# Kernel optimization log

Hardware: AMD Instinct MI355X
Metric: run time of the kernel (lower is better)

Reference implementation:

```python
import jax, jax.numpy as jnp
import numpy as np

FC = 128      # feature_channels
P = 5         # patch_size
HID = 256     # hidden
OUT = 3       # out_channels
OMEGA = 30.0  # omega_0


def _siren_linear(key, fan_in, fan_out, first=False):
    kw, kb = jax.random.split(key)
    lim = (1.0 / fan_in) if first else (np.sqrt(6.0 / fan_in) / OMEGA)
    W = jax.random.uniform(kw, (fan_in, fan_out), jnp.float32, -lim, lim)
    b = jax.random.uniform(kb, (fan_out,), jnp.float32, -lim, lim)
    return W, b


def setup_inputs() -> dict:
    key = jax.random.key(0)
    ks = jax.random.split(key, 5)
    B, H, W = 2, 128, 128
    xi = jax.random.normal(ks[0], (B, FC, H, W), jnp.float32)
    in_dim = FC * P * P + 2  # 3202 = local patch features + (x, y) coords
    W0, b0 = _siren_linear(ks[1], in_dim, HID, first=True)
    W1, b1 = _siren_linear(ks[2], HID, HID)
    W2, b2 = _siren_linear(ks[3], HID, HID)
    W3, b3 = _siren_linear(ks[4], HID, OUT)
    return {"xi": xi, "W0": W0, "b0": b0, "W1": W1, "b1": b1,
            "W2": W2, "b2": b2, "W3": W3, "b3": b3}


def reference(xi, W0, b0, W1, b1, W2, b2, W3, b3):
    B, C, H, Wd = xi.shape
    # extract_local_encoding: 5x5 local patches per pixel, zero-padded ('SAME')
    patches = jax.lax.conv_general_dilated_patches(
        xi, filter_shape=(P, P), window_strides=(1, 1), padding="SAME")  # [B, C*P*P, H, W]
    local_enc = patches.transpose(0, 2, 3, 1).reshape(B * H * Wd, C * P * P)
    # make_coords: normalized pixel coords in [-1, 1]
    ys = jnp.linspace(-1.0, 1.0, H, dtype=xi.dtype)
    xs = jnp.linspace(-1.0, 1.0, Wd, dtype=xi.dtype)
    gy, gx = jnp.meshgrid(ys, xs, indexing="ij")
    coords = jnp.stack([gx, gy], axis=-1).reshape(1, H * Wd, 2)
    coords = jnp.broadcast_to(coords, (B, H * Wd, 2)).reshape(B * H * Wd, 2)
    x = jnp.concatenate([local_enc, coords], axis=-1)  # [N, 3202]
    # SIREN MLP: sin(omega_0 * (x W + b)) for 3 layers, linear head
    h = jnp.sin(OMEGA * (x @ W0 + b0))
    h = jnp.sin(OMEGA * (h @ W1 + b1))
    h = jnp.sin(OMEGA * (h @ W2 + b2))
    out = h @ W3 + b3                                   # [N, OUT]
    return out.reshape(B, H, Wd, OUT).transpose(0, 3, 1, 2)  # [B, OUT, H, W]
```

## Files before the change

kernel.cpp:

```cpp
#include <hip/hip_runtime.h>
#include <hip/hip_bf16.h>

typedef short bf16x8 __attribute__((ext_vector_type(8)));
typedef float f32x4 __attribute__((ext_vector_type(4)));
typedef int int4v __attribute__((ext_vector_type(4)));

#define OMEGA 30.0f

__device__ __forceinline__ float fast_sin30(float z) {
  float t = z * 4.7746483f;
  t = __builtin_amdgcn_fractf(t);
  return __builtin_amdgcn_sinf(t);
}

__global__ __launch_bounds__(256) void k_prep(const float* __restrict__ xi,
                                              const float* __restrict__ W0,
                                              const float* __restrict__ W1,
                                              const float* __restrict__ W2,
                                              __hip_bfloat16* __restrict__ xt,
                                              __hip_bfloat16* __restrict__ wt2,
                                              __hip_bfloat16* __restrict__ w1t,
                                              __hip_bfloat16* __restrict__ w2t) {
  __shared__ float tile[128][33];
  int bx = blockIdx.x, t = threadIdx.x;
  if (bx < 4096) {
    int b = bx >> 11, c0 = ((bx >> 9) & 3) << 5, hw0 = (bx & 511) << 5;
    int r = t >> 5, cc = t & 31;
    const float* src = xi + (((size_t)b * 128 + c0) << 14) + hw0;
#pragma unroll
    for (int i = 0; i < 4; ++i)
      tile[r + i * 8][cc] = src[(size_t)(r + i * 8) * 16384 + cc];
    __syncthreads();
    __hip_bfloat16* dst = xt + (((size_t)b * 16384 + hw0) << 7) + c0;
#pragma unroll
    for (int i = 0; i < 4; ++i)
      dst[(size_t)(r + i * 8) * 128 + cc] = __float2bfloat16(tile[cc][r + i * 8]);
  } else if (bx < 4296) {
    int q = bx - 4096, f = q >> 3, nb = q & 7;
    int nn = t & 31, cr = t >> 5;
#pragma unroll
    for (int i = 0; i < 16; ++i) {
      int c = cr * 16 + i;
      tile[c][nn] = W0[(size_t)(c * 25 + f) * 256 + nb * 32 + nn];
    }
    __syncthreads();
#pragma unroll
    for (int i = 0; i < 16; ++i) {
      int idx = i * 256 + t;
      int n = idx >> 7, c = idx & 127;
      wt2[(size_t)f * 32768 + (size_t)(nb * 32 + n) * 128 + c] = __float2bfloat16(tile[c][n]);
    }
  } else {
    int rI = bx - 4296;
    const float* src = (rI >> 6) ? W2 : W1;
    __hip_bfloat16* dst = (rI >> 6) ? w2t : w1t;
    int k0 = ((rI >> 3) & 7) << 5, n0 = (rI & 7) << 5;
    int r = t >> 5, cc = t & 31;
#pragma unroll
    for (int i = 0; i < 4; ++i)
      tile[r + i * 8][cc] = src[(size_t)(k0 + r + i * 8) * 256 + n0 + cc];
    __syncthreads();
#pragma unroll
    for (int i = 0; i < 4; ++i)
      dst[(size_t)(n0 + r + i * 8) * 256 + k0 + cc] = __float2bfloat16(tile[cc][r + i * 8]);
  }
}

__global__ __launch_bounds__(256) void k_conv(const __hip_bfloat16* __restrict__ xt,
                                              const __hip_bfloat16* __restrict__ wt2,
                                              const float* __restrict__ W0,
                                              const float* __restrict__ b0,
                                              __hip_bfloat16* __restrict__ h0) {
  __shared__ __align__(16) char Al[240 * 128];
  __shared__ __align__(16) char Bl[2][64 * 128];
  int tid = threadIdx.x;
  int bx = blockIdx.x;
  int b = bx >> 6, tr = (bx >> 3) & 7, tc = bx & 7;
  int n0 = blockIdx.y << 6;
  int lane = tid & 63, wave = tid >> 6;
  int lr = lane & 15, lg = lane >> 4;

  float wA[4], wB[4], bb[4];
#pragma unroll
  for (int ni = 0; ni < 4; ++ni) {
    int n = n0 + (ni << 4) + lr;
    wA[ni] = W0[3200 * 256 + n];
    wB[ni] = W0[3201 * 256 + n];
    bb[ni] = b0[n];
  }

  int4v breg[2];
  auto loadB = [&](int i) {
    int cb = (i / 25) & 1, f = i % 25;
#pragma unroll
    for (int j = 0; j < 2; ++j) {
      int idx = j * 256 + tid;
      int n = idx >> 3, s = idx & 7;
      breg[j] = *(const int4v*)(wt2 + (size_t)(f * 256 + n0 + n) * 128 + cb * 64 + s * 8);
    }
  };
  auto writeB = [&](int i) {
    char* dst = Bl[i & 1];
#pragma unroll
    for (int j = 0; j < 2; ++j) {
      int idx = j * 256 + tid;
      int n = idx >> 3, s = idx & 7;
      *(int4v*)(dst + n * 128 + ((s ^ (n & 7)) << 4)) = breg[j];
    }
  };

  loadB(0);
  writeB(0);
  loadB(1);

  f32x4 acc[2][4] = {};

  for (int rh = 0; rh < 2; ++rh) {
    for (int half = 0; half < 2; ++half) {
      __syncthreads();
#pragma unroll
      for (int ii = 0; ii < 8; ++ii) {
        int idx = ii * 256 + tid;
        if (idx < 1920) {
          int pos = idx >> 3, s = idx & 7;
          int py = pos / 20, px_ = pos - py * 20;
          int gh = (tr << 4) + (rh << 3) + py - 2, gw = (tc << 4) + px_ - 2;
          int4v v = {0, 0, 0, 0};
          if ((unsigned)gh < 128u && (unsigned)gw < 128u)
            v = *(const int4v*)(xt + (((size_t)((b << 14) + (gh << 7) + gw)) << 7) + half * 64 + s * 8);
          *(int4v*)(Al + pos * 128 + ((s ^ (pos & 7)) << 4)) = v;
        }
      }
      __syncthreads();

      for (int f = 0; f < 25; ++f) {
        int i = rh * 50 + half * 25 + f;
        if (i < 99) writeB(i + 1);
        if (i < 98) loadB(i + 2);
        int fy = f / 5, fx = f - fy * 5;
        int px = lr + fx;
        char* Bbuf = Bl[i & 1];
#pragma unroll
        for (int ks = 0; ks < 2; ++ks) {
          int sk = (ks << 2) + lg;
          bf16x8 a[2], bw[4];
#pragma unroll
          for (int mi = 0; mi < 2; ++mi) {
            int fl = wave + (mi << 2);
            int pos = (fl + fy) * 20 + px;
            a[mi] = *(const bf16x8*)(Al + pos * 128 + ((sk ^ (pos & 7)) << 4));
          }
#pragma unroll
          for (int ni = 0; ni < 4; ++ni) {
            int nr = (ni << 4) + lr;
            bw[ni] = *(const bf16x8*)(Bbuf + nr * 128 + ((sk ^ (nr & 7)) << 4));
          }
#pragma unroll
          for (int mi = 0; mi < 2; ++mi)
#pragma unroll
            for (int ni = 0; ni < 4; ++ni)
              acc[mi][ni] = __builtin_amdgcn_mfma_f32_16x16x32_bf16(a[mi], bw[ni], acc[mi][ni], 0, 0, 0);
        }
        __syncthreads();
      }
    }

    char* stg = Al + wave * 4096;
#pragma unroll
    for (int mi = 0; mi < 2; ++mi) {
      int fl = wave + (mi << 2);
      int H = (tr << 4) + (rh << 3) + fl;
      float gy = -1.f + (2.f / 127.f) * (float)H;
#pragma unroll
      for (int j = 0; j < 4; ++j) {
        int cpx = (lg << 2) + j;
        int W = (tc << 4) + cpx;
        float gx = -1.f + (2.f / 127.f) * (float)W;
#pragma unroll
        for (int ni = 0; ni < 4; ++ni) {
          float v = acc[mi][ni][j] + bb[ni] + gx * wA[ni] + gy * wB[ni];
          unsigned short bits = __hip_bfloat16_raw(__float2bfloat16(fast_sin30(v))).x;
          int n = (ni << 4) + lr;
          int c = n >> 3;
          *(unsigned short*)(stg + mi * 2048 + cpx * 128 + (((c ^ (cpx & 7)) << 4) | ((n & 7) << 1))) = bits;
        }
      }
    }
#pragma unroll
    for (int mi = 0; mi < 2; ++mi) {
      int fl = wave + (mi << 2);
      int H = (tr << 4) + (rh << 3) + fl;
#pragma unroll
      for (int i2 = 0; i2 < 2; ++i2) {
        int r = (i2 << 3) + (lane >> 3);
        int c = lane & 7;
        int4v v = *(const int4v*)(stg + mi * 2048 + r * 128 + ((c ^ (r & 7)) << 4));
        int m = (b << 14) + (H << 7) + (tc << 4) + r;
        *(int4v*)(h0 + (size_t)m * 256 + n0 + c * 8) = v;
      }
    }
    if (rh == 0) {
#pragma unroll
      for (int mi = 0; mi < 2; ++mi)
#pragma unroll
        for (int ni = 0; ni < 4; ++ni)
          acc[mi][ni] = f32x4{0.f, 0.f, 0.f, 0.f};
    }
  }
}

__global__ __launch_bounds__(256, 4) void k_fused(const __hip_bfloat16* __restrict__ h0,
                                                  const __hip_bfloat16* __restrict__ w1t,
                                                  const float* __restrict__ b1,
                                                  const __hip_bfloat16* __restrict__ w2t,
                                                  const float* __restrict__ b2,
                                                  const float* __restrict__ W3,
                                                  const float* __restrict__ b3,
                                                  float* __restrict__ out) {
  __shared__ __align__(16) char Hl[32 * 512];
  __shared__ float w3l[768];
  int tid = threadIdx.x;
  int m0 = blockIdx.x << 5;
  int lane = tid & 63, wave = tid >> 6;
  int lr = lane & 15, lg = lane >> 4;
  int mg = wave >> 1, nh = wave & 1;

  for (int i = tid; i < 768; i += 256) w3l[i] = W3[i];

  int mrow = m0 + (mg << 4) + lr;
  const char* pA0 = (const char*)(h0 + ((size_t)mrow << 8)) + (lg << 4);
  const char* pB1[8];
  const char* pB2[8];
  float bb1[8], bb2[8];
#pragma unroll
  for (int ni = 0; ni < 8; ++ni) {
    int n = (nh << 7) + (ni << 4) + lr;
    pB1[ni] = (const char*)(w1t + ((size_t)n << 8)) + (lg << 4);
    pB2[ni] = (const char*)(w2t + ((size_t)n << 8)) + (lg << 4);
    bb1[ni] = b1[n];
    bb2[ni] = b2[n];
  }

  f32x4 acc[8] = {};
#pragma unroll
  for (int ks = 0; ks < 8; ++ks) {
    bf16x8 a = *(const bf16x8*)(pA0 + ks * 64);
    bf16x8 bw[8];
#pragma unroll
    for (int ni = 0; ni < 8; ++ni) bw[ni] = *(const bf16x8*)(pB1[ni] + ks * 64);
#pragma unroll
    for (int ni = 0; ni < 8; ++ni)
      acc[ni] = __builtin_amdgcn_mfma_f32_16x16x32_bf16(a, bw[ni], acc[ni], 0, 0, 0);
  }
#pragma unroll
  for (int j = 0; j < 4; ++j) {
    int r = (mg << 4) + (lg << 2) + j;
#pragma unroll
    for (int ni = 0; ni < 8; ++ni) {
      int c = (nh << 7) + (ni << 4) + lr;
      unsigned short bits =
          __hip_bfloat16_raw(__float2bfloat16(fast_sin30(acc[ni][j] + bb1[ni]))).x;
      int sl = (c >> 3) ^ (r & 31);
      *(unsigned short*)(Hl + r * 512 + (sl << 4) + ((c & 7) << 1)) = bits;
    }
  }
  __syncthreads();

  int rA = (mg << 4) + lr;
  f32x4 acc2[8] = {};
#pragma unroll
  for (int ks = 0; ks < 8; ++ks) {
    int sk = (ks << 2) + lg;
    bf16x8 a = *(const bf16x8*)(Hl + rA * 512 + ((sk ^ (rA & 31)) << 4));
    bf16x8 bw[8];
#pragma unroll
    for (int ni = 0; ni < 8; ++ni) bw[ni] = *(const bf16x8*)(pB2[ni] + ks * 64);
#pragma unroll
    for (int ni = 0; ni < 8; ++ni)
      acc2[ni] = __builtin_amdgcn_mfma_f32_16x16x32_bf16(a, bw[ni], acc2[ni], 0, 0, 0);
  }
  __syncthreads();
#pragma unroll
  for (int j = 0; j < 4; ++j) {
    int r = (mg << 4) + (lg << 2) + j;
#pragma unroll
    for (int ni = 0; ni < 8; ++ni) {
      int c = (nh << 7) + (ni << 4) + lr;
      unsigned short bits =
          __hip_bfloat16_raw(__float2bfloat16(fast_sin30(acc2[ni][j] + bb2[ni]))).x;
      int sl = (c >> 3) ^ (r & 31);
      *(unsigned short*)(Hl + r * 512 + (sl << 4) + ((c & 7) << 1)) = bits;
    }
  }
  __syncthreads();

  int pix = tid >> 3, s = tid & 7;
  float a0 = 0.f, a1 = 0.f, a2 = 0.f;
#pragma unroll
  for (int q = 0; q < 4; ++q) {
    int sl = ((s << 2) + q) ^ (pix & 31);
    bf16x8 hv = *(const bf16x8*)(Hl + pix * 512 + (sl << 4));
#pragma unroll
    for (int e = 0; e < 8; ++e) {
      int k = (s << 5) + (q << 3) + e;
      float h = __uint_as_float((unsigned)(unsigned short)hv[e] << 16);
      a0 += h * w3l[k * 3 + 0];
      a1 += h * w3l[k * 3 + 1];
      a2 += h * w3l[k * 3 + 2];
    }
  }
#pragma unroll
  for (int d = 1; d < 8; d <<= 1) {
    a0 += __shfl_xor(a0, d);
    a1 += __shfl_xor(a1, d);
    a2 += __shfl_xor(a2, d);
  }
  if (s < 3) {
    int m = m0 + pix;
    int b = m >> 14, hw = m & 16383;
    float v = (s == 0) ? (a0 + b3[0]) : (s == 1) ? (a1 + b3[1]) : (a2 + b3[2]);
    out[((b * 3 + s) << 14) + hw] = v;
  }
}

extern "C" void kernel_launch(void* const* d_in, const int* in_sizes, int n_in,
                              void* d_out, int out_size, void* d_ws, size_t ws_size,
                              hipStream_t stream) {
  const float* xi = (const float*)d_in[0];
  const float* W0 = (const float*)d_in[1];
  const float* b0 = (const float*)d_in[2];
  const float* W1 = (const float*)d_in[3];
  const float* b1 = (const float*)d_in[4];
  const float* W2 = (const float*)d_in[5];
  const float* b2 = (const float*)d_in[6];
  const float* W3 = (const float*)d_in[7];
  const float* b3 = (const float*)d_in[8];
  float* out = (float*)d_out;
  char* ws = (char*)d_ws;

  __hip_bfloat16* xt  = (__hip_bfloat16*)(ws + 0);
  __hip_bfloat16* wt2 = (__hip_bfloat16*)(ws + 8388608);
  __hip_bfloat16* w1t = (__hip_bfloat16*)(ws + 10027008);
  __hip_bfloat16* w2t = (__hip_bfloat16*)(ws + 10158080);
  __hip_bfloat16* h0  = (__hip_bfloat16*)(ws + 10289152);

  k_prep<<<4424, 256, 0, stream>>>(xi, W0, W1, W2, xt, wt2, w1t, w2t);
  k_conv<<<dim3(128, 4), 256, 0, stream>>>(xt, wt2, W0, b0, h0);
  k_fused<<<1024, 256, 0, stream>>>(h0, w1t, b1, w2t, b2, W3, b3, out);
}
```

Measured before the change: 209.3 us.

## Merge three kernels into one persistent kernel with grid-wide barriers

Replaces the prep, conv and fused-MLP launches with a single 512-block kernel whose three phases are separated by an atomic-counter grid barrier, plus a tiny init kernel that resets the barrier. Each block does 8 transpose tiles in prep, one conv tile, and two 32-row MLP tiles. The aim is to cut launch gaps and tail effects between kernels. In exchange it relies on all 512 blocks being co-resident, which deadlocks if they are not, and it spends time spinning at the barriers. The MLP phase also loses the occupancy hint it had before, and the shared-memory footprint is sized for the largest phase.

```diff
diff --git a/kernel.cpp b/kernel.cpp
--- a/kernel.cpp
+++ b/kernel.cpp
@@ -6,6 +6,7 @@
 typedef int int4v __attribute__((ext_vector_type(4)));
 
 #define OMEGA 30.0f
+#define NBLK 512
 
 __device__ __forceinline__ float fast_sin30(float z) {
   float t = z * 4.7746483f;
@@ -13,313 +14,349 @@
   return __builtin_amdgcn_sinf(t);
 }
 
-__global__ __launch_bounds__(256) void k_prep(const float* __restrict__ xi,
+__device__ __forceinline__ void gbar(int* bar, int& mygen) {
+  __syncthreads();
+  if (threadIdx.x == 0) {
+    int g = mygen + 1;
+    if (__hip_atomic_fetch_add(&bar[0], 1, __ATOMIC_ACQ_REL, __HIP_MEMORY_SCOPE_AGENT) == NBLK - 1) {
+      __hip_atomic_store(&bar[0], 0, __ATOMIC_RELAXED, __HIP_MEMORY_SCOPE_AGENT);
+      __hip_atomic_store(&bar[16], g, __ATOMIC_RELEASE, __HIP_MEMORY_SCOPE_AGENT);
+    } else {
+      while (__hip_atomic_load(&bar[16], __ATOMIC_ACQUIRE, __HIP_MEMORY_SCOPE_AGENT) < g)
+        __builtin_amdgcn_s_sleep(2);
+    }
+    mygen = g;
+  }
+  __syncthreads();
+}
+
+__global__ void k_init(int* bar) {
+  bar[0] = 0;
+  bar[16] = 0;
+}
+
+__global__ __launch_bounds__(256) void k_mega(const float* __restrict__ xi,
                                               const float* __restrict__ W0,
+                                              const float* __restrict__ b0,
+                                              const float* __restrict__ b1,
+                                              const float* __restrict__ b2,
+                                              const float* __restrict__ W3,
+                                              const float* __restrict__ b3,
                                               const float* __restrict__ W1,
                                               const float* __restrict__ W2,
                                               __hip_bfloat16* __restrict__ xt,
                                               __hip_bfloat16* __restrict__ wt2,
                                               __hip_bfloat16* __restrict__ w1t,
-                                              __hip_bfloat16* __restrict__ w2t) {
-  __shared__ float tile[128][33];
-  int bx = blockIdx.x, t = threadIdx.x;
-  if (bx < 4096) {
-    int b = bx >> 11, c0 = ((bx >> 9) & 3) << 5, hw0 = (bx & 511) << 5;
-    int r = t >> 5, cc = t & 31;
-    const float* src = xi + (((size_t)b * 128 + c0) << 14) + hw0;
-#pragma unroll
-    for (int i = 0; i < 4; ++i)
-      tile[r + i * 8][cc] = src[(size_t)(r + i * 8) * 16384 + cc];
+                                              __hip_bfloat16* __restrict__ w2t,
+                                              __hip_bfloat16* __restrict__ h0,
+                                              float* __restrict__ out,
+                                              int* bar) {
+  __shared__ __align__(16) char SMEM[47104];
+  int bid = blockIdx.x;
+  int tid = threadIdx.x;
+  int mygen = 0;
+
+  {
+    float(*tile)[33] = reinterpret_cast<float(*)[33]>(SMEM);
+    int r = tid >> 5, cc = tid & 31;
+    for (int i8 = 0; i8 < 8; ++i8) {
+      int bx = (bid << 3) + i8;
+      int b = bx >> 11, c0 = ((bx >> 9) & 3) << 5, hw0 = (bx & 511) << 5;
+      const float* src = xi + (((size_t)b * 128 + c0) << 14) + hw0;
+      float v[4];
+#pragma unroll
+      for (int i = 0; i < 4; ++i) v[i] = src[(size_t)(r + i * 8) * 16384 + cc];
+      __syncthreads();
+#pragma unroll
+      for (int i = 0; i < 4; ++i) tile[r + i * 8][cc] = v[i];
+      __syncthreads();
+      __hip_bfloat16* dst = xt + (((size_t)b * 16384 + hw0) << 7) + c0;
+#pragma unroll
+      for (int i = 0; i < 4; ++i)
+        dst[(size_t)(r + i * 8) * 128 + cc] = __float2bfloat16(tile[cc][r + i * 8]);
+    }
     __syncthreads();
-    __hip_bfloat16* dst = xt + (((size_t)b * 16384 + hw0) << 7) + c0;
-#pragma unroll
-    for (int i = 0; i < 4; ++i)
-      dst[(size_t)(r + i * 8) * 128 + cc] = __float2bfloat16(tile[cc][r + i * 8]);
-  } else if (bx < 4296) {
-    int q = bx - 4096, f = q >> 3, nb = q & 7;
-    int nn = t & 31, cr = t >> 5;
-#pragma unroll
-    for (int i = 0; i < 16; ++i) {
-      int c = cr * 16 + i;
-      tile[c][nn] = W0[(size_t)(c * 25 + f) * 256 + nb * 32 + nn];
-    }
-    __syncthreads();
-#pragma unroll
-    for (int i = 0; i < 16; ++i) {
-      int idx = i * 256 + t;
-      int n = idx >> 7, c = idx & 127;
-      wt2[(size_t)f * 32768 + (size_t)(nb * 32 + n) * 128 + c] = __float2bfloat16(tile[c][n]);
-    }
-  } else {
-    int rI = bx - 4296;
-    const float* src = (rI >> 6) ? W2 : W1;
-    __hip_bfloat16* dst = (rI >> 6) ? w2t : w1t;
-    int k0 = ((rI >> 3) & 7) << 5, n0 = (rI & 7) << 5;
-    int r = t >> 5, cc = t & 31;
-#pragma unroll
-    for (int i = 0; i < 4; ++i)
-      tile[r + i * 8][cc] = src[(size_t)(k0 + r + i * 8) * 256 + n0 + cc];
-    __syncthreads();
-#pragma unroll
-    for (int i = 0; i < 4; ++i)
-      dst[(size_t)(n0 + r + i * 8) * 256 + k0 + cc] = __float2bfloat16(tile[cc][r + i * 8]);
+    if (bid < 200) {
+      int f = bid >> 3, nb = bid & 7;
+      int nn = tid & 31, cr = tid >> 5;
+#pragma unroll
+      for (int i = 0; i < 16; ++i) {
+        int c = cr * 16 + i;
+        tile[c][nn] = W0[(size_t)(c * 25 + f) * 256 + nb * 32 + nn];
+      }
+      __syncthreads();
+#pragma unroll
+      for (int i = 0; i < 16; ++i) {
+        int idx = i * 256 + tid;
+        int n = idx >> 7, c = idx & 127;
+        wt2[(size_t)f * 32768 + (size_t)(nb * 32 + n) * 128 + c] = __float2bfloat16(tile[c][n]);
+      }
+    } else if (bid < 328) {
+      int rI = bid - 200;
+      const float* src = (rI >> 6) ? W2 : W1;
+      __hip_bfloat16* dst = (rI >> 6) ? w2t : w1t;
+      int k0 = ((rI >> 3) & 7) << 5, n0 = (rI & 7) << 5;
+#pragma unroll
+      for (int i = 0; i < 4; ++i)
+        tile[r + i * 8][cc] = src[(size_t)(k0 + r + i * 8) * 256 + n0 + cc];
+      __syncthreads();
+#pragma unroll
+      for (int i = 0; i < 4; ++i)
+        dst[(size_t)(n0 + r + i * 8) * 256 + k0 + cc] = __float2bfloat16(tile[cc][r + i * 8]);
+    }
   }
-}
-
-__global__ __launch_bounds__(256) void k_conv(const __hip_bfloat16* __restrict__ xt,
-                                              const __hip_bfloat16* __restrict__ wt2,
-                                              const float* __restrict__ W0,
-                                              const float* __restrict__ b0,
-                                              __hip_bfloat16* __restrict__ h0) {
-  __shared__ __align__(16) char Al[240 * 128];
-  __shared__ __align__(16) char Bl[2][64 * 128];
-  int tid = threadIdx.x;
-  int bx = blockIdx.x;
-  int b = bx >> 6, tr = (bx >> 3) & 7, tc = bx & 7;
-  int n0 = blockIdx.y << 6;
-  int lane = tid & 63, wave = tid >> 6;
-  int lr = lane & 15, lg = lane >> 4;
-
-  float wA[4], wB[4], bb[4];
-#pragma unroll
-  for (int ni = 0; ni < 4; ++ni) {
-    int n = n0 + (ni << 4) + lr;
-    wA[ni] = W0[3200 * 256 + n];
-    wB[ni] = W0[3201 * 256 + n];
-    bb[ni] = b0[n];
+
+  gbar(bar, mygen);
+
+  {
+    char* Al = SMEM;
+    char* Bl = SMEM + 30720;
+    int bx = bid & 127;
+    int b = bx >> 6, tr = (bx >> 3) & 7, tc = bx & 7;
+    int n0 = (bid >> 7) << 6;
+    int lane = tid & 63, wave = tid >> 6;
+    int lr = lane & 15, lg = lane >> 4;
+
+    float wA[4], wB[4], bb[4];
+#pragma unroll
+    for (int ni = 0; ni < 4; ++ni) {
+      int n = n0 + (ni << 4) + lr;
+      wA[ni] = W0[3200 * 256 + n];
+      wB[ni] = W0[3201 * 256 + n];
+      bb[ni] = b0[n];
+    }
+
+    int4v breg[2];
+    auto loadB = [&](int i) {
+      int cb = (i / 25) & 1, f = i % 25;
+#pragma unroll
+      for (int j = 0; j < 2; ++j) {
+        int idx = j * 256 + tid;
+        int n = idx >> 3, s = idx & 7;
+        breg[j] = *(const int4v*)(wt2 + (size_t)(f * 256 + n0 + n) * 128 + cb * 64 + s * 8);
+      }
+    };
+    auto writeB = [&](int i) {
+      char* dst = Bl + (i & 1) * 8192;
+#pragma unroll
+      for (int j = 0; j < 2; ++j) {
+        int idx = j * 256 + tid;
+        int n = idx >> 3, s = idx & 7;
+        *(int4v*)(dst + n * 128 + ((s ^ (n & 7)) << 4)) = breg[j];
+      }
+    };
+
+    loadB(0);
+    writeB(0);
+    loadB(1);
+
+    f32x4 acc[2][4] = {};
+
+    for (int rh = 0; rh < 2; ++rh) {
+      for (int half = 0; half < 2; ++half) {
+        __syncthreads();
+#pragma unroll
+        for (int ii = 0; ii < 8; ++ii) {
+          int idx = ii * 256 + tid;
+          if (idx < 1920) {
+            int pos = idx >> 3, s = idx & 7;
+            int py = pos / 20, px_ = pos - py * 20;
+            int gh = (tr << 4) + (rh << 3) + py - 2, gw = (tc << 4) + px_ - 2;
+            int4v v = {0, 0, 0, 0};
+            if ((unsigned)gh < 128u && (unsigned)gw < 128u)
+              v = *(const int4v*)(xt + (((size_t)((b << 14) + (gh << 7) + gw)) << 7) + half * 64 + s * 8);
+            *(int4v*)(Al + pos * 128 + ((s ^ (pos & 7)) << 4)) = v;
+          }
+        }
+        __syncthreads();
+
+        for (int f = 0; f < 25; ++f) {
+          int i = rh * 50 + half * 25 + f;
+          if (i < 99) writeB(i + 1);
+          if (i < 98) loadB(i + 2);
+          int fy = f / 5, fx = f - fy * 5;
+          int px = lr + fx;
+          char* Bbuf = Bl + (i & 1) * 8192;
+#pragma unroll
+          for (int ks = 0; ks < 2; ++ks) {
+            int sk = (ks << 2) + lg;
+            bf16x8 a[2], bw[4];
+#pragma unroll
+            for (int mi = 0; mi < 2; ++mi) {
+              int fl = wave + (mi << 2);
+              int pos = (fl + fy) * 20 + px;
+              a[mi] = *(const bf16x8*)(Al + pos * 128 + ((sk ^ (pos & 7)) << 4));
+            }
+#pragma unroll
+            for (int ni = 0; ni < 4; ++ni) {
+              int nr = (ni << 4) + lr;
+              bw[ni] = *(const bf16x8*)(Bbuf + nr * 128 + ((sk ^ (nr & 7)) << 4));
+            }
+#pragma unroll
+            for (int mi = 0; mi < 2; ++mi)
+#pragma unroll
+              for (int ni = 0; ni < 4; ++ni)
+                acc[mi][ni] = __builtin_amdgcn_mfma_f32_16x16x32_bf16(a[mi], bw[ni], acc[mi][ni], 0, 0, 0);
+          }
+          __syncthreads();
+        }
+      }
+
+      char* stg = Al + wave * 4096;
+#pragma unroll
+      for (int mi = 0; mi < 2; ++mi) {
+        int fl = wave + (mi << 2);
+        int H = (tr << 4) + (rh << 3) + fl;
+        float gy = -1.f + (2.f / 127.f) * (float)H;
+#pragma unroll
+        for (int j = 0; j < 4; ++j) {
+          int cpx = (lg << 2) + j;
+          int W = (tc << 4) + cpx;
+          float gx = -1.f + (2.f / 127.f) * (float)W;
+#pragma unroll
+          for (int ni = 0; ni < 4; ++ni) {
+            float v = acc[mi][ni][j] + bb[ni] + gx * wA[ni] + gy * wB[ni];
+            unsigned short bits = __hip_bfloat16_raw(__float2bfloat16(fast_sin30(v))).x;
+            int n = (ni << 4) + lr;
+            int c = n >> 3;
+            *(unsigned short*)(stg + mi * 2048 + cpx * 128 + (((c ^ (cpx & 7)) << 4) | ((n & 7) << 1))) = bits;
+          }
+        }
+      }
+#pragma unroll
+      for (int mi = 0; mi < 2; ++mi) {
+        int fl = wave + (mi << 2);
+        int H = (tr << 4) + (rh << 3) + fl;
+#pragma unroll
+        for (int i2 = 0; i2 < 2; ++i2) {
+          int r2 = (i2 << 3) + (lane >> 3);
+          int c = lane & 7;
+          int4v v = *(const int4v*)(stg + mi * 2048 + r2 * 128 + ((c ^ (r2 & 7)) << 4));
+          int m = (b << 14) + (H << 7) + (tc << 4) + r2;
+          *(int4v*)(h0 + (size_t)m * 256 + n0 + c * 8) = v;
+        }
+      }
+      if (rh == 0) {
+#pragma unroll
+        for (int mi = 0; mi < 2; ++mi)
+#pragma unroll
+          for (int ni = 0; ni < 4; ++ni)
+            acc[mi][ni] = f32x4{0.f, 0.f, 0.f, 0.f};
+      }
+    }
   }
 
-  int4v breg[2];
-  auto loadB = [&](int i) {
-    int cb = (i / 25) & 1, f = i % 25;
-#pragma unroll
-    for (int j = 0; j < 2; ++j) {
-      int idx = j * 256 + tid;
-      int n = idx >> 3, s = idx & 7;
-      breg[j] = *(const int4v*)(wt2 + (size_t)(f * 256 + n0 + n) * 128 + cb * 64 + s * 8);
-    }
-  };
-  auto writeB = [&](int i) {
-    char* dst = Bl[i & 1];
-#pragma unroll
-    for (int j = 0; j < 2; ++j) {
-      int idx = j * 256 + tid;
-      int n = idx >> 3, s = idx & 7;
-      *(int4v*)(dst + n * 128 + ((s ^ (n & 7)) << 4)) = breg[j];
-    }
-  };
-
-  loadB(0);
-  writeB(0);
-  loadB(1);
-
-  f32x4 acc[2][4] = {};
-
-  for (int rh = 0; rh < 2; ++rh) {
-    for (int half = 0; half < 2; ++half) {
-      __syncthreads();
-#pragma unroll
-      for (int ii = 0; ii < 8; ++ii) {
-        int idx = ii * 256 + tid;
-        if (idx < 1920) {
-          int pos = idx >> 3, s = idx & 7;
-          int py = pos / 20, px_ = pos - py * 20;
-          int gh = (tr << 4) + (rh << 3) + py - 2, gw = (tc << 4) + px_ - 2;
-          int4v v = {0, 0, 0, 0};
-          if ((unsigned)gh < 128u && (unsigned)gw < 128u)
-            v = *(const int4v*)(xt + (((size_t)((b << 14) + (gh << 7) + gw)) << 7) + half * 64 + s * 8);
-          *(int4v*)(Al + pos * 128 + ((s ^ (pos & 7)) << 4)) = v;
-        }
-      }
-      __syncthreads();
-
-      for (int f = 0; f < 25; ++f) {
-        int i = rh * 50 + half * 25 + f;
-        if (i < 99) writeB(i + 1);
-        if (i < 98) loadB(i + 2);
-        int fy = f / 5, fx = f - fy * 5;
-        int px = lr + fx;
-        char* Bbuf = Bl[i & 1];
-#pragma unroll
-        for (int ks = 0; ks < 2; ++ks) {
-          int sk = (ks << 2) + lg;
-          bf16x8 a[2], bw[4];
-#pragma unroll
-          for (int mi = 0; mi < 2; ++mi) {
-            int fl = wave + (mi << 2);
-            int pos = (fl + fy) * 20 + px;
-            a[mi] = *(const bf16x8*)(Al + pos * 128 + ((sk ^ (pos & 7)) << 4));
-          }
-#pragma unroll
-          for (int ni = 0; ni < 4; ++ni) {
-            int nr = (ni << 4) + lr;
-            bw[ni] = *(const bf16x8*)(Bbuf + nr * 128 + ((sk ^ (nr & 7)) << 4));
-          }
-#pragma unroll
-          for (int mi = 0; mi < 2; ++mi)
-#pragma unroll
-            for (int ni = 0; ni < 4; ++ni)
-              acc[mi][ni] = __builtin_amdgcn_mfma_f32_16x16x32_bf16(a[mi], bw[ni], acc[mi][ni], 0, 0, 0);
-        }
-        __syncthreads();
-      }
-    }
-
-    char* stg = Al + wave * 4096;
-#pragma unroll
-    for (int mi = 0; mi < 2; ++mi) {
-      int fl = wave + (mi << 2);
-      int H = (tr << 4) + (rh << 3) + fl;
-      float gy = -1.f + (2.f / 127.f) * (float)H;
+  gbar(bar, mygen);
+
+  {
+    char* Hl = SMEM;
+    float* w3l = (float*)(SMEM + 16384);
+    int lane = tid & 63, wave = tid >> 6;
+    int lr = lane & 15, lg = lane >> 4;
+    int mg = wave >> 1, nh = wave & 1;
+
+    for (int i = tid; i < 768; i += 256) w3l[i] = W3[i];
+
+    const char* pB1[8];
+    const char* pB2[8];
+    float bb1[8], bb2[8];
+#pragma unroll
+    for (int ni = 0; ni < 8; ++ni) {
+      int n = (nh << 7) + (ni << 4) + lr;
+      pB1[ni] = (const char*)(w1t + ((size_t)n << 8)) + (lg << 4);
+      pB2[ni] = (const char*)(w2t + ((size_t)n << 8)) + (lg << 4);
+      bb1[ni] = b1[n];
+      bb2[ni] = b2[n];
+    }
+
+    for (int u = 0; u < 2; ++u) {
+      int m0 = ((bid << 1) + u) << 5;
+      __syncthreads();
+
+      int mrow = m0 + (mg << 4) + lr;
+      const char* pA0 = (const char*)(h0 + ((size_t)mrow << 8)) + (lg << 4);
+
+      f32x4 acc[8] = {};
+#pragma unroll
+      for (int ks = 0; ks < 8; ++ks) {
+        bf16x8 a = *(const bf16x8*)(pA0 + ks * 64);
+        bf16x8 bw[8];
+#pragma unroll
+        for (int ni = 0; ni < 8; ++ni) bw[ni] = *(const bf16x8*)(pB1[ni] + ks * 64);
+#pragma unroll
+        for (int ni = 0; ni < 8; ++ni)
+          acc[ni] = __builtin_amdgcn_mfma_f32_16x16x32_bf16(a, bw[ni], acc[ni], 0, 0, 0);
+      }
 #pragma unroll
       for (int j = 0; j < 4; ++j) {
-        int cpx = (lg << 2) + j;
-        int W = (tc << 4) + cpx;
-        float gx = -1.f + (2.f / 127.f) * (float)W;
-#pragma unroll
-        for (int ni = 0; ni < 4; ++ni) {
-          float v = acc[mi][ni][j] + bb[ni] + gx * wA[ni] + gy * wB[ni];
-          unsigned short bits = __hip_bfloat16_raw(__float2bfloat16(fast_sin30(v))).x;
-          int n = (ni << 4) + lr;
-          int c = n >> 3;
-          *(unsigned short*)(stg + mi * 2048 + cpx * 128 + (((c ^ (cpx & 7)) << 4) | ((n & 7) << 1))) = bits;
-        }
-      }
-    }
-#pragma unroll
-    for (int mi = 0; mi < 2; ++mi) {
-      int fl = wave + (mi << 2);
-      int H = (tr << 4) + (rh << 3) + fl;
-#pragma unroll
-      for (int i2 = 0; i2 < 2; ++i2) {
-        int r = (i2 << 3) + (lane >> 3);
-        int c = lane & 7;
-        int4v v = *(const int4v*)(stg + mi * 2048 + r * 128 + ((c ^ (r & 7)) << 4));
-        int m = (b << 14) + (H << 7) + (tc << 4) + r;
-        *(int4v*)(h0 + (size_t)m * 256 + n0 + c * 8) = v;
-      }
-    }
-    if (rh == 0) {
-#pragma unroll
-      for (int mi = 0; mi < 2; ++mi)
-#pragma unroll
-        for (int ni = 0; ni < 4; ++ni)
-          acc[mi][ni] = f32x4{0.f, 0.f, 0.f, 0.f};
-    }
-  }
-}
-
-__global__ __launch_bounds__(256, 4) void k_fused(const __hip_bfloat16* __restrict__ h0,
-                                                  const __hip_bfloat16* __restrict__ w1t,
-                                                  const float* __restrict__ b1,
-                                                  const __hip_bfloat16* __restrict__ w2t,
-                                                  const float* __restrict__ b2,
-                                                  const float* __restrict__ W3,
-                                                  const float* __restrict__ b3,
-                                                  float* __restrict__ out) {
-  __shared__ __align__(16) char Hl[32 * 512];
-  __shared__ float w3l[768];
-  int tid = threadIdx.x;
-  int m0 = blockIdx.x << 5;
-  int lane = tid & 63, wave = tid >> 6;
-  int lr = lane & 15, lg = lane >> 4;
-  int mg = wave >> 1, nh = wave & 1;
-
-  for (int i = tid; i < 768; i += 256) w3l[i] = W3[i];
-
-  int mrow = m0 + (mg << 4) + lr;
-  const char* pA0 = (const char*)(h0 + ((size_t)mrow << 8)) + (lg << 4);
-  const char* pB1[8];
-  const char* pB2[8];
-  float bb1[8], bb2[8];
-#pragma unroll
-  for (int ni = 0; ni < 8; ++ni) {
-    int n = (nh << 7) + (ni << 4) + lr;
-    pB1[ni] = (const char*)(w1t + ((size_t)n << 8)) + (lg << 4);
-    pB2[ni] = (const char*)(w2t + ((size_t)n << 8)) + (lg << 4);
-    bb1[ni] = b1[n];
-    bb2[ni] = b2[n];
-  }
-
-  f32x4 acc[8] = {};
-#pragma unroll
-  for (int ks = 0; ks < 8; ++ks) {
-    bf16x8 a = *(const bf16x8*)(pA0 + ks * 64);
-    bf16x8 bw[8];
-#pragma unroll
-    for (int ni = 0; ni < 8; ++ni) bw[ni] = *(const bf16x8*)(pB1[ni] + ks * 64);
-#pragma unroll
-    for (int ni = 0; ni < 8; ++ni)
-      acc[ni] = __builtin_amdgcn_mfma_f32_16x16x32_bf16(a, bw[ni], acc[ni], 0, 0, 0);
-  }
-#pragma unroll
-  for (int j = 0; j < 4; ++j) {
-    int r = (mg << 4) + (lg << 2) + j;
-#pragma unroll
-    for (int ni = 0; ni < 8; ++ni) {
-      int c = (nh << 7) + (ni << 4) + lr;
-      unsigned short bits =
-          __hip_bfloat16_raw(__float2bfloat16(fast_sin30(acc[ni][j] + bb1[ni]))).x;
-      int sl = (c >> 3) ^ (r & 31);
-      *(unsigned short*)(Hl + r * 512 + (sl << 4) + ((c & 7) << 1)) = bits;
-    }
-  }
-  __syncthreads();
-
-  int rA = (mg << 4) + lr;
-  f32x4 acc2[8] = {};
-#pragma unroll
-  for (int ks = 0; ks < 8; ++ks) {
-    int sk = (ks << 2) + lg;
-    bf16x8 a = *(const bf16x8*)(Hl + rA * 512 + ((sk ^ (rA & 31)) << 4));
-    bf16x8 bw[8];
-#pragma unroll
-    for (int ni = 0; ni < 8; ++ni) bw[ni] = *(const bf16x8*)(pB2[ni] + ks * 64);
-#pragma unroll
-    for (int ni = 0; ni < 8; ++ni)
-      acc2[ni] = __builtin_amdgcn_mfma_f32_16x16x32_bf16(a, bw[ni], acc2[ni], 0, 0, 0);
-  }
-  __syncthreads();
-#pragma unroll
-  for (int j = 0; j < 4; ++j) {
-    int r = (mg << 4) + (lg << 2) + j;
-#pragma unroll
-    for (int ni = 0; ni < 8; ++ni) {
-      int c = (nh << 7) + (ni << 4) + lr;
-      unsigned short bits =
-          __hip_bfloat16_raw(__float2bfloat16(fast_sin30(acc2[ni][j] + bb2[ni]))).x;
-      int sl = (c >> 3) ^ (r & 31);
-      *(unsigned short*)(Hl + r * 512 + (sl << 4) + ((c & 7) << 1)) = bits;
-    }
-  }
-  __syncthreads();
-
-  int pix = tid >> 3, s = tid & 7;
-  float a0 = 0.f, a1 = 0.f, a2 = 0.f;
-#pragma unroll
-  for (int q = 0; q < 4; ++q) {
-    int sl = ((s << 2) + q) ^ (pix & 31);
-    bf16x8 hv = *(const bf16x8*)(Hl + pix * 512 + (sl << 4));
-#pragma unroll
-    for (int e = 0; e < 8; ++e) {
-      int k = (s << 5) + (q << 3) + e;
-      float h = __uint_as_float((unsigned)(unsigned short)hv[e] << 16);
-      a0 += h * w3l[k * 3 + 0];
-      a1 += h * w3l[k * 3 + 1];
-      a2 += h * w3l[k * 3 + 2];
-    }
-  }
-#pragma unroll
-  for (int d = 1; d < 8; d <<= 1) {
-    a0 += __shfl_xor(a0, d);
-    a1 += __shfl_xor(a1, d);
-    a2 += __shfl_xor(a2, d);
-  }
-  if (s < 3) {
-    int m = m0 + pix;
-    int b = m >> 14, hw = m & 16383;
-    float v = (s == 0) ? (a0 + b3[0]) : (s == 1) ? (a1 + b3[1]) : (a2 + b3[2]);
-    out[((b * 3 + s) << 14) + hw] = v;
+        int r = (mg << 4) + (lg << 2) + j;
+#pragma unroll
+        for (int ni = 0; ni < 8; ++ni) {
+          int c = (nh << 7) + (ni << 4) + lr;
+          unsigned short bits =
+              __hip_bfloat16_raw(__float2bfloat16(fast_sin30(acc[ni][j] + bb1[ni]))).x;
+          int sl = (c >> 3) ^ (r & 31);
+          *(unsigned short*)(Hl + r * 512 + (sl << 4) + ((c & 7) << 1)) = bits;
+        }
+      }
+      __syncthreads();
+
+      int rA = (mg << 4) + lr;
+      f32x4 acc2[8] = {};
+#pragma unroll
+      for (int ks = 0; ks < 8; ++ks) {
+        int sk = (ks << 2) + lg;
+        bf16x8 a = *(const bf16x8*)(Hl + rA * 512 + ((sk ^ (rA & 31)) << 4));
+        bf16x8 bw[8];
+#pragma unroll
+        for (int ni = 0; ni < 8; ++ni) bw[ni] = *(const bf16x8*)(pB2[ni] + ks * 64);
+#pragma unroll
+        for (int ni = 0; ni < 8; ++ni)
+          acc2[ni] = __builtin_amdgcn_mfma_f32_16x16x32_bf16(a, bw[ni], acc2[ni], 0, 0, 0);
+      }
+      __syncthreads();
+#pragma unroll
+      for (int j = 0; j < 4; ++j) {
+        int r = (mg << 4) + (lg << 2) + j;
+#pragma unroll
+        for (int ni = 0; ni < 8; ++ni) {
+          int c = (nh << 7) + (ni << 4) + lr;
+          unsigned short bits =
+              __hip_bfloat16_raw(__float2bfloat16(fast_sin30(acc2[ni][j] + bb2[ni]))).x;
+          int sl = (c >> 3) ^ (r & 31);
+          *(unsigned short*)(Hl + r * 512 + (sl << 4) + ((c & 7) << 1)) = bits;
+        }
+      }
+      __syncthreads();
+
+      int pix = tid >> 3, s = tid & 7;
+      float a0 = 0.f, a1 = 0.f, a2 = 0.f;
+#pragma unroll
+      for (int q = 0; q < 4; ++q) {
+        int sl = ((s << 2) + q) ^ (pix & 31);
+        bf16x8 hv = *(const bf16x8*)(Hl + pix * 512 + (sl << 4));
+#pragma unroll
+        for (int e = 0; e < 8; ++e) {
+          int k = (s << 5) + (q << 3) + e;
+          float h = __uint_as_float((unsigned)(unsigned short)hv[e] << 16);
+          a0 += h * w3l[k * 3 + 0];
+          a1 += h * w3l[k * 3 + 1];
+          a2 += h * w3l[k * 3 + 2];
+        }
+      }
+#pragma unroll
+      for (int d = 1; d < 8; d <<= 1) {
+        a0 += __shfl_xor(a0, d);
+        a1 += __shfl_xor(a1, d);
+        a2 += __shfl_xor(a2, d);
+      }
+      if (s < 3) {
+        int m = m0 + pix;
+        int b = m >> 14, hw = m & 16383;
+        float v = (s == 0) ? (a0 + b3[0]) : (s == 1) ? (a1 + b3[1]) : (a2 + b3[2]);
+        out[((b * 3 + s) << 14) + hw] = v;
+      }
+    }
   }
 }
 
@@ -343,8 +380,9 @@
   __hip_bfloat16* w1t = (__hip_bfloat16*)(ws + 10027008);
   __hip_bfloat16* w2t = (__hip_bfloat16*)(ws + 10158080);
   __hip_bfloat16* h0  = (__hip_bfloat16*)(ws + 10289152);
-
-  k_prep<<<4424, 256, 0, stream>>>(xi, W0, W1, W2, xt, wt2, w1t, w2t);
-  k_conv<<<dim3(128, 4), 256, 0, stream>>>(xt, wt2, W0, b0, h0);
-  k_fused<<<1024, 256, 0, stream>>>(h0, w1t, b1, w2t, b2, W3, b3, out);
-}
+  int* bar            = (int*)(ws + 27066368);
+
+  k_init<<<1, 1, 0, stream>>>(bar);
+  k_mega<<<NBLK, 256, 0, stream>>>(xi, W0, b0, b1, b2, W3, b3, W1, W2,
+                                   xt, wt2, w1t, w2t, h0, out, bar);
+}
```

Result: slower. 352.2 us (+68.3%).

## Stage two filter taps per barrier in conv and vectorize prep transposes

Applied to the files above, without the earlier changes.

The conv kernel now loads and double-buffers the B weights for two filter taps per pipeline step, which halves the number of __syncthreads barriers in the inner loop at the cost of doubling the B LDS buffer. The prep kernel handles all 128 channels per block and writes 16-byte bf16x8 vectors instead of scalar bf16 stores. This cuts its grid from 4424 to 1352 blocks and coalesces its writes. The tap-pair indexing uses multiply-shift divisions, and the odd final tap of each 25-tap group is handled separately.

```diff
diff --git a/kernel.cpp b/kernel.cpp
--- a/kernel.cpp
+++ b/kernel.cpp
@@ -11,6 +11,10 @@
   float t = z * 4.7746483f;
   t = __builtin_amdgcn_fractf(t);
   return __builtin_amdgcn_sinf(t);
+}
+
+__device__ __forceinline__ unsigned short f2bf(float x) {
+  return __hip_bfloat16_raw(__float2bfloat16(x)).x;
 }
 
 __global__ __launch_bounds__(256) void k_prep(const float* __restrict__ xi,
@@ -21,48 +25,61 @@
                                               __hip_bfloat16* __restrict__ wt2,
                                               __hip_bfloat16* __restrict__ w1t,
                                               __hip_bfloat16* __restrict__ w2t) {
-  __shared__ float tile[128][33];
-  int bx = blockIdx.x, t = threadIdx.x;
-  if (bx < 4096) {
-    int b = bx >> 11, c0 = ((bx >> 9) & 3) << 5, hw0 = (bx & 511) << 5;
-    int r = t >> 5, cc = t & 31;
-    const float* src = xi + (((size_t)b * 128 + c0) << 14) + hw0;
-#pragma unroll
-    for (int i = 0; i < 4; ++i)
-      tile[r + i * 8][cc] = src[(size_t)(r + i * 8) * 16384 + cc];
-    __syncthreads();
-    __hip_bfloat16* dst = xt + (((size_t)b * 16384 + hw0) << 7) + c0;
-#pragma unroll
-    for (int i = 0; i < 4; ++i)
-      dst[(size_t)(r + i * 8) * 128 + cc] = __float2bfloat16(tile[cc][r + i * 8]);
-  } else if (bx < 4296) {
-    int q = bx - 4096, f = q >> 3, nb = q & 7;
-    int nn = t & 31, cr = t >> 5;
+  __shared__ float lds[128][33];
+  int bid = blockIdx.x, t = threadIdx.x;
+  if (bid < 1024) {
+    int b = bid >> 9, hw0 = (bid & 511) << 5;
+    int cc = t & 31, cr = t >> 5;
 #pragma unroll
     for (int i = 0; i < 16; ++i) {
       int c = cr * 16 + i;
-      tile[c][nn] = W0[(size_t)(c * 25 + f) * 256 + nb * 32 + nn];
-    }
-    __syncthreads();
+      lds[c][cc] = xi[(((size_t)(b * 128 + c)) << 14) + hw0 + cc];
+    }
+    __syncthreads();
+    int cg = t & 15;
+#pragma unroll
+    for (int it = 0; it < 2; ++it) {
+      int hw = (t >> 4) + (it << 4);
+      bf16x8 v;
+#pragma unroll
+      for (int w = 0; w < 8; ++w) v[w] = (short)f2bf(lds[cg * 8 + w][hw]);
+      *(bf16x8*)(xt + (((size_t)((b << 14) + hw0 + hw)) << 7) + cg * 8) = v;
+    }
+  } else if (bid < 1224) {
+    int q = bid - 1024, f = q >> 3, nb = q & 7;
+    int nn = t & 31, cr = t >> 5;
 #pragma unroll
     for (int i = 0; i < 16; ++i) {
-      int idx = i * 256 + t;
-      int n = idx >> 7, c = idx & 127;
-      wt2[(size_t)f * 32768 + (size_t)(nb * 32 + n) * 128 + c] = __float2bfloat16(tile[c][n]);
+      int c = cr * 16 + i;
+      lds[c][nn] = W0[(size_t)(c * 25 + f) * 256 + nb * 32 + nn];
+    }
+    __syncthreads();
+    int cg = t & 15;
+#pragma unroll
+    for (int it = 0; it < 2; ++it) {
+      int n = (t >> 4) + (it << 4);
+      bf16x8 v;
+#pragma unroll
+      for (int w = 0; w < 8; ++w) v[w] = (short)f2bf(lds[cg * 8 + w][n]);
+      *(bf16x8*)(wt2 + (size_t)f * 32768 + (size_t)(nb * 32 + n) * 128 + cg * 8) = v;
     }
   } else {
-    int rI = bx - 4296;
+    int rI = bid - 1224;
     const float* src = (rI >> 6) ? W2 : W1;
     __hip_bfloat16* dst = (rI >> 6) ? w2t : w1t;
     int k0 = ((rI >> 3) & 7) << 5, n0 = (rI & 7) << 5;
-    int r = t >> 5, cc = t & 31;
+    int cc = t & 31, r = t >> 5;
 #pragma unroll
     for (int i = 0; i < 4; ++i)
-      tile[r + i * 8][cc] = src[(size_t)(k0 + r + i * 8) * 256 + n0 + cc];
-    __syncthreads();
-#pragma unroll
-    for (int i = 0; i < 4; ++i)
-      dst[(size_t)(n0 + r + i * 8) * 256 + k0 + cc] = __float2bfloat16(tile[cc][r + i * 8]);
+      lds[r + i * 8][cc] = src[(size_t)(k0 + r + i * 8) * 256 + n0 + cc];
+    __syncthreads();
+    if (t < 128) {
+      int kg = t & 3, n = t >> 2;
+      bf16x8 v;
+#pragma unroll
+      for (int w = 0; w < 8; ++w) v[w] = (short)f2bf(lds[kg * 8 + w][n]);
+      *(bf16x8*)(dst + (size_t)(n0 + n) * 256 + k0 + kg * 8) = v;
+    }
   }
 }
 
@@ -72,7 +89,7 @@
                                               const float* __restrict__ b0,
                                               __hip_bfloat16* __restrict__ h0) {
   __shared__ __align__(16) char Al[240 * 128];
-  __shared__ __align__(16) char Bl[2][64 * 128];
+  __shared__ __align__(16) char Bl[2][2 * 64 * 128];
   int tid = threadIdx.x;
   int bx = blockIdx.x;
   int b = bx >> 6, tr = (bx >> 3) & 7, tc = bx & 7;
@@ -89,23 +106,43 @@
     bb[ni] = b0[n];
   }
 
-  int4v breg[2];
-  auto loadB = [&](int i) {
-    int cb = (i / 25) & 1, f = i % 25;
-#pragma unroll
-    for (int j = 0; j < 2; ++j) {
-      int idx = j * 256 + tid;
-      int n = idx >> 3, s = idx & 7;
-      breg[j] = *(const int4v*)(wt2 + (size_t)(f * 256 + n0 + n) * 128 + cb * 64 + s * 8);
-    }
+  int4v breg[4];
+  auto loadB = [&](int p) {
+    int q = (p * 5) >> 6, j = p - q * 13;
+    int f0 = j * 2, cb = q & 1;
+    int n = tid >> 3, s = tid & 7;
+#pragma unroll
+    for (int jj = 0; jj < 2; ++jj) {
+      int idx = jj * 256 + tid;
+      int nn = idx >> 3, ss = idx & 7;
+      breg[jj] = *(const int4v*)(wt2 + (size_t)(f0 * 256 + n0 + nn) * 128 + cb * 64 + ss * 8);
+    }
+    if (j < 12) {
+#pragma unroll
+      for (int jj = 0; jj < 2; ++jj) {
+        int idx = jj * 256 + tid;
+        int nn = idx >> 3, ss = idx & 7;
+        breg[2 + jj] = *(const int4v*)(wt2 + (size_t)((f0 + 1) * 256 + n0 + nn) * 128 + cb * 64 + ss * 8);
+      }
+    }
+    (void)n; (void)s;
   };
-  auto writeB = [&](int i) {
-    char* dst = Bl[i & 1];
-#pragma unroll
-    for (int j = 0; j < 2; ++j) {
-      int idx = j * 256 + tid;
-      int n = idx >> 3, s = idx & 7;
-      *(int4v*)(dst + n * 128 + ((s ^ (n & 7)) << 4)) = breg[j];
+  auto writeB = [&](int p) {
+    int q = (p * 5) >> 6, j = p - q * 13;
+    char* dst = Bl[p & 1];
+#pragma unroll
+    for (int jj = 0; jj < 2; ++jj) {
+      int idx = jj * 256 + tid;
+      int nn = idx >> 3, ss = idx & 7;
+      *(int4v*)(dst + nn * 128 + ((ss ^ (nn & 7)) << 4)) = breg[jj];
+    }
+    if (j < 12) {
+#pragma unroll
+      for (int jj = 0; jj < 2; ++jj) {
+        int idx = jj * 256 + tid;
+        int nn = idx >> 3, ss = idx & 7;
+        *(int4v*)(dst + 8192 + nn * 128 + ((ss ^ (nn & 7)) << 4)) = breg[2 + jj];
+      }
     }
   };
 
@@ -115,31 +152,36 @@
 
   f32x4 acc[2][4] = {};
 
-  for (int rh = 0; rh < 2; ++rh) {
-    for (int half = 0; half < 2; ++half) {
-      __syncthreads();
-#pragma unroll
-      for (int ii = 0; ii < 8; ++ii) {
-        int idx = ii * 256 + tid;
-        if (idx < 1920) {
-          int pos = idx >> 3, s = idx & 7;
-          int py = pos / 20, px_ = pos - py * 20;
-          int gh = (tr << 4) + (rh << 3) + py - 2, gw = (tc << 4) + px_ - 2;
-          int4v v = {0, 0, 0, 0};
-          if ((unsigned)gh < 128u && (unsigned)gw < 128u)
-            v = *(const int4v*)(xt + (((size_t)((b << 14) + (gh << 7) + gw)) << 7) + half * 64 + s * 8);
-          *(int4v*)(Al + pos * 128 + ((s ^ (pos & 7)) << 4)) = v;
-        }
-      }
-      __syncthreads();
-
-      for (int f = 0; f < 25; ++f) {
-        int i = rh * 50 + half * 25 + f;
-        if (i < 99) writeB(i + 1);
-        if (i < 98) loadB(i + 2);
-        int fy = f / 5, fx = f - fy * 5;
+  for (int q = 0; q < 4; ++q) {
+    int rh = q >> 1, half = q & 1;
+    __syncthreads();
+#pragma unroll
+    for (int ii = 0; ii < 8; ++ii) {
+      int idx = ii * 256 + tid;
+      if (idx < 1920) {
+        int pos = idx >> 3, s = idx & 7;
+        int py = pos / 20, px_ = pos - py * 20;
+        int gh = (tr << 4) + (rh << 3) + py - 2, gw = (tc << 4) + px_ - 2;
+        int4v v = {0, 0, 0, 0};
+        if ((unsigned)gh < 128u && (unsigned)gw < 128u)
+          v = *(const int4v*)(xt + (((size_t)((b << 14) + (gh << 7) + gw)) << 7) + half * 64 + s * 8);
+        *(int4v*)(Al + pos * 128 + ((s ^ (pos & 7)) << 4)) = v;
+      }
+    }
+    __syncthreads();
+
+    for (int j = 0; j < 13; ++j) {
+      int p = q * 13 + j;
+      if (p < 51) writeB(p + 1);
+      if (p < 50) loadB(p + 2);
+      int f0 = j * 2;
+      int cnt = (j == 12) ? 1 : 2;
+      char* base = Bl[p & 1];
+      for (int ft = 0; ft < cnt; ++ft) {
+        int f = f0 + ft;
+        int fy = (f * 13) >> 6, fx = f - fy * 5;
         int px = lr + fx;
-        char* Bbuf = Bl[i & 1];
+        char* Bbuf = base + ft * 8192;
 #pragma unroll
         for (int ks = 0; ks < 2; ++ks) {
           int sk = (ks << 2) + lg;
@@ -161,50 +203,52 @@
             for (int ni = 0; ni < 4; ++ni)
               acc[mi][ni] = __builtin_amdgcn_mfma_f32_16x16x32_bf16(a[mi], bw[ni], acc[mi][ni], 0, 0, 0);
         }
-        __syncthreads();
-      }
-    }
-
-    char* stg = Al + wave * 4096;
-#pragma unroll
-    for (int mi = 0; mi < 2; ++mi) {
-      int fl = wave + (mi << 2);
-      int H = (tr << 4) + (rh << 3) + fl;
-      float gy = -1.f + (2.f / 127.f) * (float)H;
-#pragma unroll
-      for (int j = 0; j < 4; ++j) {
-        int cpx = (lg << 2) + j;
-        int W = (tc << 4) + cpx;
-        float gx = -1.f + (2.f / 127.f) * (float)W;
-#pragma unroll
-        for (int ni = 0; ni < 4; ++ni) {
-          float v = acc[mi][ni][j] + bb[ni] + gx * wA[ni] + gy * wB[ni];
-          unsigned short bits = __hip_bfloat16_raw(__float2bfloat16(fast_sin30(v))).x;
-          int n = (ni << 4) + lr;
-          int c = n >> 3;
-          *(unsigned short*)(stg + mi * 2048 + cpx * 128 + (((c ^ (cpx & 7)) << 4) | ((n & 7) << 1))) = bits;
+      }
+      __syncthreads();
+    }
+
+    if (half == 1) {
+      char* stg = Al + wave * 4096;
+#pragma unroll
+      for (int mi = 0; mi < 2; ++mi) {
+        int fl = wave + (mi << 2);
+        int H = (tr << 4) + (rh << 3) + fl;
+        float gy = -1.f + (2.f / 127.f) * (float)H;
+#pragma unroll
+        for (int j = 0; j < 4; ++j) {
+          int cpx = (lg << 2) + j;
+          int W = (tc << 4) + cpx;
+          float gx = -1.f + (2.f / 127.f) * (float)W;
+#pragma unroll
+          for (int ni = 0; ni < 4; ++ni) {
+            float v = acc[mi][ni][j] + bb[ni] + gx * wA[ni] + gy * wB[ni];
+            unsigned short bits = f2bf(fast_sin30(v));
+            int n = (ni << 4) + lr;
+            int c = n >> 3;
+            *(unsigned short*)(stg + mi * 2048 + cpx * 128 + (((c ^ (cpx & 7)) << 4) | ((n & 7) << 1))) = bits;
+          }
         }
       }
-    }
-#pragma unroll
-    for (int mi = 0; mi < 2; ++mi) {
-      int fl = wave + (mi << 2);
-      int H = (tr << 4) + (rh << 3) + fl;
-#pragma unroll
-      for (int i2 = 0; i2 < 2; ++i2) {
-        int r = (i2 << 3) + (lane >> 3);
-        int c = lane & 7;
-        int4v v = *(const int4v*)(stg + mi * 2048 + r * 128 + ((c ^ (r & 7)) << 4));
-        int m = (b << 14) + (H << 7) + (tc << 4) + r;
-        *(int4v*)(h0 + (size_t)m * 256 + n0 + c * 8) = v;
-      }
-    }
-    if (rh == 0) {
-#pragma unroll
-      for (int mi = 0; mi < 2; ++mi)
-#pragma unroll
-        for (int ni = 0; ni < 4; ++ni)
-          acc[mi][ni] = f32x4{0.f, 0.f, 0.f, 0.f};
+#pragma unroll
+      for (int mi = 0; mi < 2; ++mi) {
+        int fl = wave + (mi << 2);
+        int H = (tr << 4) + (rh << 3) + fl;
+#pragma unroll
+        for (int i2 = 0; i2 < 2; ++i2) {
+          int r2 = (i2 << 3) + (lane >> 3);
+          int c = lane & 7;
+          int4v v = *(const int4v*)(stg + mi * 2048 + r2 * 128 + ((c ^ (r2 & 7)) << 4));
+          int m = (b << 14) + (H << 7) + (tc << 4) + r2;
+          *(int4v*)(h0 + (size_t)m * 256 + n0 + c * 8) = v;
+        }
+      }
+      if (rh == 0) {
+#pragma unroll
+        for (int mi = 0; mi < 2; ++mi)
+#pragma unroll
+          for (int ni = 0; ni < 4; ++ni)
+            acc[mi][ni] = f32x4{0.f, 0.f, 0.f, 0.f};
+      }
     }
   }
 }
@@ -258,8 +302,7 @@
 #pragma unroll
     for (int ni = 0; ni < 8; ++ni) {
       int c = (nh << 7) + (ni << 4) + lr;
-      unsigned short bits =
-          __hip_bfloat16_raw(__float2bfloat16(fast_sin30(acc[ni][j] + bb1[ni]))).x;
+      unsigned short bits = f2bf(fast_sin30(acc[ni][j] + bb1[ni]));
       int sl = (c >> 3) ^ (r & 31);
       *(unsigned short*)(Hl + r * 512 + (sl << 4) + ((c & 7) << 1)) = bits;
     }
@@ -286,8 +329,7 @@
 #pragma unroll
     for (int ni = 0; ni < 8; ++ni) {
       int c = (nh << 7) + (ni << 4) + lr;
-      unsigned short bits =
-          __hip_bfloat16_raw(__float2bfloat16(fast_sin30(acc2[ni][j] + bb2[ni]))).x;
+      unsigned short bits = f2bf(fast_sin30(acc2[ni][j] + bb2[ni]));
       int sl = (c >> 3) ^ (r & 31);
       *(unsigned short*)(Hl + r * 512 + (sl << 4) + ((c & 7) << 1)) = bits;
     }
@@ -344,7 +386,7 @@
   __hip_bfloat16* w2t = (__hip_bfloat16*)(ws + 10158080);
   __hip_bfloat16* h0  = (__hip_bfloat16*)(ws + 10289152);
 
-  k_prep<<<4424, 256, 0, stream>>>(xi, W0, W1, W2, xt, wt2, w1t, w2t);
+  k_prep<<<1352, 256, 0, stream>>>(xi, W0, W1, W2, xt, wt2, w1t, w2t);
   k_conv<<<dim3(128, 4), 256, 0, stream>>>(xt, wt2, W0, b0, h0);
   k_fused<<<1024, 256, 0, stream>>>(h0, w1t, b1, w2t, b2, W3, b3, out);
 }
```

New measurement: 204.7 us. 2.2% less time.
